# Performance work log

Hardware: AMD Instinct MI355X
Metric: run time of the kernel (lower is better)

## Reference

```python
import jax, jax.numpy as jnp
import numpy as np

N = 50000        # nodes
E = 800000       # edges (avg degree 16)
C_PREV = 256
HID = 256        # C * 4, C = 64
ALPHA = 0.1      # GCNII-style initial-residual weight
LAMBDA = 0.5     # identity-mapping hyperparameter
LAYER = 1
BN_EPS = 1e-5
GIN_EPS = 0.0    # GIN epsilon (default 0)


def setup_inputs() -> dict:
    key = jax.random.key(0)
    ks = jax.random.split(key, 6)
    s0 = jax.random.normal(ks[0], (N, C_PREV), jnp.float32)
    s1 = jax.random.normal(ks[1], (N, C_PREV), jnp.float32)
    x_0 = jax.random.normal(ks[2], (N, HID), jnp.float32)
    # preprocess MLP: Linear(C_prev -> 4C, bias=False) + BatchNorm + ReLU
    W_pre = jax.random.normal(ks[3], (C_PREV, HID), jnp.float32) / np.sqrt(C_PREV).astype(np.float32)
    gamma = jnp.ones((HID,), jnp.float32)
    beta_bn = jnp.zeros((HID,), jnp.float32)
    # ginii op weight (identity-mapped linear, GCNII style)
    W_op = jax.random.normal(ks[4], (HID, HID), jnp.float32) / np.sqrt(HID).astype(np.float32)
    edge_index = jax.random.randint(ks[5], (2, E), 0, N, dtype=jnp.int32)
    return {"s0": s0, "s1": s1, "x_0": x_0, "W_pre": W_pre, "gamma": gamma,
            "beta_bn": beta_bn, "W_op": W_op, "edge_index": edge_index,
            "drop_prob": 0, "training": 0}


def reference(s0, s1, x_0, W_pre, gamma, beta_bn, W_op, edge_index, drop_prob, training):
    # preprocess1: Linear (no bias) -> BatchNorm (batch stats) -> ReLU
    h = s1 @ W_pre                                        # [N, HID]
    mu = h.mean(axis=0)
    var = h.var(axis=0)
    h = (h - mu) * jax.lax.rsqrt(var + BN_EPS) * gamma + beta_bn
    h = jax.nn.relu(h)

    # ginii: GIN-style sum aggregation over edge_index with initial residual
    # and identity-mapped weight (GCNII trick).
    src, dst = edge_index[0], edge_index[1]
    agg = jax.ops.segment_sum(h[src], dst, num_segments=N)   # [N, HID]
    h = (1.0 + GIN_EPS) * h + agg
    support = (1.0 - ALPHA) * h + ALPHA * x_0
    beta = float(np.log(LAMBDA / LAYER + 1.0))
    out = jax.nn.relu((1.0 - beta) * support + beta * (support @ W_op))
    return out
```

## Files before the change

kernel.cpp:

```cpp
#include <hip/hip_runtime.h>

#define NNODES 50000
#define NEDGES 800000
#define HIDDIM 256
#define NCHUNK  1563
#define GEMMB   256
#define DEGCAP  64

constexpr float kAlpha = 0.1f;
constexpr float kBnEps = 1e-5f;
constexpr float kBeta  = 0.40546510810816438198f;

typedef __attribute__((ext_vector_type(8))) short  bf16x8;
typedef __attribute__((ext_vector_type(4))) float  f32x4;

typedef __attribute__((address_space(1))) const unsigned int gu32;
typedef __attribute__((address_space(3))) unsigned int       lu32;

static __device__ __forceinline__ unsigned short f2bf(float f) {
  unsigned u = __float_as_uint(f);
  u = (u + 0x7FFFu + ((u >> 16) & 1u)) >> 16;
  return (unsigned short)u;
}
static __device__ __forceinline__ float bf2f(unsigned short h) {
  return __uint_as_float(((unsigned)h) << 16);
}

static __device__ __forceinline__ void load_B_transpose(
    const float* __restrict__ W, unsigned short* Bl, int t) {
#pragma unroll 4
  for (int i = 0; i < 128; ++i) {
    int idx = i * 512 + t;
    int k = idx >> 8, n = idx & 255;
    unsigned short w = f2bf(W[k * 256 + n]);
    *(unsigned short*)((char*)Bl + n * 512 + ((k * 2) ^ ((n & 7) << 4))) = w;
  }
}

__global__ __launch_bounds__(512) void gemm1_fill_persist_k(
    const float* __restrict__ Ain,
    const float* __restrict__ W_pre,
    unsigned short* __restrict__ Cout,
    float* __restrict__ colsum,
    float* __restrict__ colsumsq,
    const int* __restrict__ ei,
    int* __restrict__ cnt,
    int* __restrict__ esrc,
    int M) {
  __shared__ __align__(16) unsigned short Bl[256 * 256];
  __shared__ __align__(16) unsigned short Al[2][32 * 256];

  const int t    = threadIdx.x;
  const int lane = t & 63;
  const int wid  = t >> 6;
  const int wr   = wid >> 2;
  const int wc   = wid & 3;

  load_B_transpose(W_pre, Bl, t);

  float spart[4] = {0.f, 0.f, 0.f, 0.f};
  float qpart[4] = {0.f, 0.f, 0.f, 0.f};

  auto stageA = [&](int buf, int chunk) {
    const int r0 = chunk * 32;
#pragma unroll
    for (int s = 0; s < 4; ++s) {
      int e   = s * 512 + t;
      int row = e >> 6;
      int c4  = e & 63;
      int arow = r0 + row;
      float4 p = make_float4(0.f, 0.f, 0.f, 0.f);
      if (arow < M) p = *(const float4*)(Ain + (size_t)arow * 256 + c4 * 4);
      short4 v;
      v.x = (short)f2bf(p.x); v.y = (short)f2bf(p.y);
      v.z = (short)f2bf(p.z); v.w = (short)f2bf(p.w);
      char* base = (char*)&Al[buf][0] + row * 512;
      *(short4*)(base + ((c4 * 8) ^ ((row & 7) << 4))) = v;
    }
  };

  stageA(0, blockIdx.x);
  __syncthreads();

  const int4* src4 = (const int4*)ei;
  const int4* dst4 = (const int4*)(ei + NEDGES);
  const int n4 = NEDGES / 4;

  int nc = 0;
  for (int c = blockIdx.x; c < NCHUNK; c += GEMMB, ++nc) {
    const int cur = nc & 1;
    const int cn = c + GEMMB;
    if (cn < NCHUNK) stageA(cur ^ 1, cn);

    if (nc < 2) {
      int i = nc * (GEMMB * 512) + (int)blockIdx.x * 512 + t;
      if (i < n4) {
        int4 s = src4[i];
        int4 d = dst4[i];
        int p;
        p = atomicAdd(&cnt[d.x], 1); if (p < DEGCAP) esrc[d.x * DEGCAP + p] = s.x;
        p = atomicAdd(&cnt[d.y], 1); if (p < DEGCAP) esrc[d.y * DEGCAP + p] = s.y;
        p = atomicAdd(&cnt[d.z], 1); if (p < DEGCAP) esrc[d.z * DEGCAP + p] = s.z;
        p = atomicAdd(&cnt[d.w], 1); if (p < DEGCAP) esrc[d.w * DEGCAP + p] = s.w;
      }
    }

    f32x4 acc[4] = {};
    const int arow_f = wr * 16 + (lane & 15);
    const int asw = (arow_f & 7) << 4;
#pragma unroll
    for (int ks = 0; ks < 8; ++ks) {
      const int koff = ks * 64 + ((lane >> 4) * 16);
      bf16x8 af = *(const bf16x8*)((char*)&Al[cur][0] + arow_f * 512 + (koff ^ asw));
#pragma unroll
      for (int n = 0; n < 4; ++n) {
        int nr = wc * 64 + n * 16 + (lane & 15);
        bf16x8 bfr = *(const bf16x8*)((char*)Bl + (size_t)nr * 512 + (koff ^ ((nr & 7) << 4)));
        acc[n] = __builtin_amdgcn_mfma_f32_16x16x32_bf16(af, bfr, acc[n], 0, 0, 0);
      }
    }

#pragma unroll
    for (int n = 0; n < 4; ++n) {
      int col = wc * 64 + n * 16 + (lane & 15);
      float s = 0.f, q = 0.f;
#pragma unroll
      for (int r = 0; r < 4; ++r) {
        int row = c * 32 + wr * 16 + (lane >> 4) * 4 + r;
        float v = acc[n][r];
        s += v; q += v * v;
        if (row < M) Cout[(size_t)row * 256 + col] = f2bf(v);
      }
      spart[n] += s; qpart[n] += q;
    }
    __syncthreads();
  }

#pragma unroll
  for (int n = 0; n < 4; ++n) {
    float s = spart[n], q = qpart[n];
    s += __shfl_xor(s, 16); s += __shfl_xor(s, 32);
    q += __shfl_xor(q, 16); q += __shfl_xor(q, 32);
    if (lane < 16) {
      int col = wc * 64 + n * 16 + lane;
      atomicAdd(&colsum[col], s);
      atomicAdd(&colsumsq[col], q);
    }
  }
}

__global__ __launch_bounds__(512) void gemm2_persist_k(
    const unsigned short* __restrict__ Ain,
    const float* __restrict__ W_op,
    float* __restrict__ Cout,
    int M) {
  __shared__ __align__(16) unsigned short Bl[256 * 256];
  __shared__ __align__(16) unsigned short Al[2][32 * 256];

  const int t    = threadIdx.x;
  const int lane = t & 63;
  const int wid  = t >> 6;
  const int wr   = wid >> 2;
  const int wc   = wid & 3;

  load_B_transpose(W_op, Bl, t);

  auto stageA = [&](int buf, int chunk) {
    const int lrow = lane >> 5, lchk = lane & 31;
#pragma unroll
    for (int c = 0; c < 2; ++c) {
      int issue = wid * 2 + c;
      int row = issue * 2 + lrow;
      int srcoff = (lchk * 16) ^ ((row & 7) << 4);
      const char* g = (const char*)Ain + (size_t)(chunk * 32 + row) * 512 + srcoff;
      char* l = (char*)&Al[buf][0] + issue * 1024 + lane * 16;
      __builtin_amdgcn_global_load_lds((gu32*)g, (lu32*)l, 16, 0, 0);
    }
  };

  stageA(0, blockIdx.x);
  __syncthreads();

  int nc = 0;
  for (int c = blockIdx.x; c < NCHUNK; c += GEMMB, ++nc) {
    const int cur = nc & 1;
    if (c + GEMMB < NCHUNK) stageA(cur ^ 1, c + GEMMB);

    f32x4 acc[4] = {};
    const int arow_f = wr * 16 + (lane & 15);
    const int asw = (arow_f & 7) << 4;
#pragma unroll
    for (int ks = 0; ks < 8; ++ks) {
      const int koff = ks * 64 + ((lane >> 4) * 16);
      bf16x8 af = *(const bf16x8*)((char*)&Al[cur][0] + arow_f * 512 + (koff ^ asw));
#pragma unroll
      for (int n = 0; n < 4; ++n) {
        int nr = wc * 64 + n * 16 + (lane & 15);
        bf16x8 bfr = *(const bf16x8*)((char*)Bl + (size_t)nr * 512 + (koff ^ ((nr & 7) << 4)));
        acc[n] = __builtin_amdgcn_mfma_f32_16x16x32_bf16(af, bfr, acc[n], 0, 0, 0);
      }
    }

#pragma unroll
    for (int n = 0; n < 4; ++n) {
      int col = wc * 64 + n * 16 + (lane & 15);
#pragma unroll
      for (int r = 0; r < 4; ++r) {
        int rl = wr * 16 + (lane >> 4) * 4 + r;
        int row = c * 32 + rl;
        if (row < M) {
          unsigned short sv = *(const unsigned short*)
              ((char*)&Al[cur][0] + rl * 512 + ((col * 2) ^ ((rl & 7) << 4)));
          Cout[(size_t)row * 256 + col] =
              fmaxf((1.f - kBeta) * bf2f(sv) + kBeta * acc[n][r], 0.f);
        }
      }
    }
    __syncthreads();
  }
}

__global__ __launch_bounds__(256) void agg_bn_support_k(
    const unsigned short* __restrict__ hb,
    const int* __restrict__ cnt,
    const int* __restrict__ esrc,
    const float* __restrict__ x0,
    const float* __restrict__ colsum,
    const float* __restrict__ colsumsq,
    const float* __restrict__ gamma,
    const float* __restrict__ beta_bn,
    unsigned short* __restrict__ supp_bf) {
  __shared__ float s_sc[256], s_sh[256];
  {
    int j = threadIdx.x;
    float inv_n = 1.0f / (float)NNODES;
    float mu  = colsum[j] * inv_n;
    float var = colsumsq[j] * inv_n - mu * mu;
    float rstd = rsqrtf(var + kBnEps);
    float g = gamma[j] * rstd;
    s_sc[j] = g;
    s_sh[j] = beta_bn[j] - mu * g;
  }
  __syncthreads();

  const int hw   = threadIdx.x >> 5;
  const int lane = threadIdx.x & 31;
  const int d    = blockIdx.x * 8 + hw;
  const int off  = lane * 8;

  float sc[8], sh[8];
  *(float4*)&sc[0] = *(const float4*)(s_sc + off);
  *(float4*)&sc[4] = *(const float4*)(s_sc + off + 4);
  *(float4*)&sh[0] = *(const float4*)(s_sh + off);
  *(float4*)&sh[4] = *(const float4*)(s_sh + off + 4);

  const int beg = d * DEGCAP;
  int deg = cnt[d]; if (deg > DEGCAP) deg = DEGCAP;
  const int end = beg + deg;
  float acc[8] = {0.f, 0.f, 0.f, 0.f, 0.f, 0.f, 0.f, 0.f};

  for (int bb = beg; bb < end; bb += 32) {
    int c32 = end - bb; if (c32 > 32) c32 = 32;
    int myi = esrc[bb + ((lane < c32) ? lane : 0)];
    int u = 0;
    for (; u + 3 < c32; u += 4) {
      int s0 = __shfl(myi, u, 32),     s1 = __shfl(myi, u + 1, 32);
      int s2 = __shfl(myi, u + 2, 32), s3 = __shfl(myi, u + 3, 32);
      bf16x8 v0 = *(const bf16x8*)(hb + (size_t)s0 * HIDDIM + off);
      bf16x8 v1 = *(const bf16x8*)(hb + (size_t)s1 * HIDDIM + off);
      bf16x8 v2 = *(const bf16x8*)(hb + (size_t)s2 * HIDDIM + off);
      bf16x8 v3 = *(const bf16x8*)(hb + (size_t)s3 * HIDDIM + off);
#pragma unroll
      for (int j = 0; j < 8; ++j) {
        acc[j] += fmaxf(fmaf(bf2f((unsigned short)v0[j]), sc[j], sh[j]), 0.f)
                + fmaxf(fmaf(bf2f((unsigned short)v1[j]), sc[j], sh[j]), 0.f)
                + fmaxf(fmaf(bf2f((unsigned short)v2[j]), sc[j], sh[j]), 0.f)
                + fmaxf(fmaf(bf2f((unsigned short)v3[j]), sc[j], sh[j]), 0.f);
      }
    }
    for (; u < c32; ++u) {
      int s0 = __shfl(myi, u, 32);
      bf16x8 v0 = *(const bf16x8*)(hb + (size_t)s0 * HIDDIM + off);
#pragma unroll
      for (int j = 0; j < 8; ++j)
        acc[j] += fmaxf(fmaf(bf2f((unsigned short)v0[j]), sc[j], sh[j]), 0.f);
    }
  }

  bf16x8 vd = *(const bf16x8*)(hb + (size_t)d * HIDDIM + off);
  f32x4 xa = __builtin_nontemporal_load((const f32x4*)(x0 + (size_t)d * HIDDIM + off));
  f32x4 xb = __builtin_nontemporal_load((const f32x4*)(x0 + (size_t)d * HIDDIM + off + 4));
  float xs[8] = {xa.x, xa.y, xa.z, xa.w, xb.x, xb.y, xb.z, xb.w};
  bf16x8 o;
#pragma unroll
  for (int j = 0; j < 8; ++j) {
    float hv = fmaxf(fmaf(bf2f((unsigned short)vd[j]), sc[j], sh[j]), 0.f);
    o[j] = (short)f2bf((1.f - kAlpha) * (hv + acc[j]) + kAlpha * xs[j]);
  }
  __builtin_nontemporal_store(o, (bf16x8*)(supp_bf + (size_t)d * HIDDIM + off));
}

extern "C" void kernel_launch(void* const* d_in, const int* in_sizes, int n_in,
                              void* d_out, int out_size, void* d_ws, size_t ws_size,
                              hipStream_t stream) {
  const float* s1    = (const float*)d_in[1];
  const float* x0    = (const float*)d_in[2];
  const float* W_pre = (const float*)d_in[3];
  const float* gamma = (const float*)d_in[4];
  const float* betab = (const float*)d_in[5];
  const float* W_op  = (const float*)d_in[6];
  const int*   ei    = (const int*)d_in[7];
  float* out = (float*)d_out;

  const size_t NH = (size_t)NNODES * HIDDIM;
  unsigned short* hbf   = (unsigned short*)d_ws;
  unsigned short* supbf = hbf + NH;
  int*   cnt      = (int*)(supbf + NH);
  float* colsum   = (float*)(cnt + NNODES);
  float* colsumsq = colsum + HIDDIM;
  int*   esrc     = (int*)(colsumsq + HIDDIM);

  hipMemsetAsync(cnt, 0, (NNODES + 2 * HIDDIM) * sizeof(int), stream);

  gemm1_fill_persist_k<<<GEMMB, 512, 0, stream>>>(s1, W_pre, hbf, colsum, colsumsq,
                                                  ei, cnt, esrc, NNODES);

  agg_bn_support_k<<<(NNODES + 7) / 8, 256, 0, stream>>>(hbf, cnt, esrc, x0,
                                                         colsum, colsumsq, gamma, betab,
                                                         supbf);

  gemm2_persist_k<<<GEMMB, 512, 0, stream>>>(supbf, W_op, out, NNODES);
}
```

Baseline: 174.2 us.

## Split gemm1 into dynamic-scheduled MFMA waves plus dedicated edge-fill warps

Replaces the persistent gemm1 kernel with a 768-thread block in which 8 waves pull 16-row chunks from a global atomic work counter. Each wave loads its A fragments straight from global memory into registers and computes all 256 columns. The other 4 waves do the CSR-style edge bucketing at the same time. Column sums are gathered in LDS atomics before one global atomic per column. The aim is to balance work across blocks, overlap edge filling with the GEMM, and drop the LDS staging of A. The cost is more register pressure (16 accumulators) and no double buffering of A loads.

```diff
diff --git a/kernel.cpp b/kernel.cpp
--- a/kernel.cpp
+++ b/kernel.cpp
@@ -4,6 +4,7 @@
 #define NEDGES 800000
 #define HIDDIM 256
 #define NCHUNK  1563
+#define NCH16   3125
 #define GEMMB   256
 #define DEGCAP  64
 
@@ -24,6 +25,106 @@
 }
 static __device__ __forceinline__ float bf2f(unsigned short h) {
   return __uint_as_float(((unsigned)h) << 16);
+}
+
+__global__ __launch_bounds__(768) void gemm1_fill_k(
+    const float* __restrict__ Ain,
+    const float* __restrict__ W_pre,
+    unsigned short* __restrict__ Cout,
+    float* __restrict__ colsum,
+    float* __restrict__ colsumsq,
+    const int* __restrict__ ei,
+    int* __restrict__ cnt,
+    int* __restrict__ esrc,
+    int* __restrict__ chunkctr) {
+  __shared__ __align__(16) unsigned short Bl[256 * 256];
+  __shared__ float csl[256], cql[256];
+
+  const int t    = threadIdx.x;
+  const int lane = t & 63;
+  const int wid  = t >> 6;
+
+  for (int idx = t; idx < 65536; idx += 768) {
+    int k = idx >> 8, n = idx & 255;
+    unsigned short w = f2bf(W_pre[k * 256 + n]);
+    *(unsigned short*)((char*)Bl + n * 512 + ((k * 2) ^ ((n & 7) << 4))) = w;
+  }
+  if (t < 256) { csl[t] = 0.f; cql[t] = 0.f; }
+  __syncthreads();
+
+  if (wid < 8) {
+    while (true) {
+      int c0;
+      if (lane == 0) c0 = atomicAdd(chunkctr, 1);
+      c0 = __shfl(c0, 0);
+      if (c0 >= NCH16) break;
+
+      const float* ap = Ain + (size_t)(c0 * 16 + (lane & 15)) * 256 + ((lane >> 4) * 8);
+      bf16x8 af[8];
+#pragma unroll
+      for (int ks = 0; ks < 8; ++ks) {
+        float4 p0 = *(const float4*)(ap + ks * 32);
+        float4 p1 = *(const float4*)(ap + ks * 32 + 4);
+        bf16x8 v;
+        v[0] = (short)f2bf(p0.x); v[1] = (short)f2bf(p0.y);
+        v[2] = (short)f2bf(p0.z); v[3] = (short)f2bf(p0.w);
+        v[4] = (short)f2bf(p1.x); v[5] = (short)f2bf(p1.y);
+        v[6] = (short)f2bf(p1.z); v[7] = (short)f2bf(p1.w);
+        af[ks] = v;
+      }
+
+      f32x4 acc[16] = {};
+#pragma unroll
+      for (int ks = 0; ks < 8; ++ks) {
+        const int koff = ks * 64 + ((lane >> 4) * 16);
+#pragma unroll
+        for (int n = 0; n < 16; ++n) {
+          int nr = n * 16 + (lane & 15);
+          bf16x8 bfr = *(const bf16x8*)((char*)Bl + (size_t)nr * 512 + (koff ^ ((nr & 7) << 4)));
+          acc[n] = __builtin_amdgcn_mfma_f32_16x16x32_bf16(af[ks], bfr, acc[n], 0, 0, 0);
+        }
+      }
+
+#pragma unroll
+      for (int n = 0; n < 16; ++n) {
+        int col = n * 16 + (lane & 15);
+        float s = 0.f, q = 0.f;
+#pragma unroll
+        for (int r = 0; r < 4; ++r) {
+          int orow = c0 * 16 + (lane >> 4) * 4 + r;
+          float v = acc[n][r];
+          s += v; q += v * v;
+          Cout[(size_t)orow * 256 + col] = f2bf(v);
+        }
+        s += __shfl_xor(s, 16); s += __shfl_xor(s, 32);
+        q += __shfl_xor(q, 16); q += __shfl_xor(q, 32);
+        if (lane < 16) {
+          atomicAdd(&csl[col], s);
+          atomicAdd(&cql[col], q);
+        }
+      }
+    }
+  } else {
+    const int4* src4 = (const int4*)ei;
+    const int4* dst4 = (const int4*)(ei + NEDGES);
+    const int n4 = NEDGES / 4;
+    int ft = (int)blockIdx.x * 256 + (t - 512);
+    for (int i = ft; i < n4; i += GEMMB * 256) {
+      int4 s = src4[i];
+      int4 d = dst4[i];
+      int p;
+      p = atomicAdd(&cnt[d.x], 1); if (p < DEGCAP) esrc[d.x * DEGCAP + p] = s.x;
+      p = atomicAdd(&cnt[d.y], 1); if (p < DEGCAP) esrc[d.y * DEGCAP + p] = s.y;
+      p = atomicAdd(&cnt[d.z], 1); if (p < DEGCAP) esrc[d.z * DEGCAP + p] = s.z;
+      p = atomicAdd(&cnt[d.w], 1); if (p < DEGCAP) esrc[d.w * DEGCAP + p] = s.w;
+    }
+  }
+
+  __syncthreads();
+  if (t < 256) {
+    atomicAdd(&colsum[t], csl[t]);
+    atomicAdd(&colsumsq[t], cql[t]);
+  }
 }
 
 static __device__ __forceinline__ void load_B_transpose(
@@ -34,118 +135,6 @@
     int k = idx >> 8, n = idx & 255;
     unsigned short w = f2bf(W[k * 256 + n]);
     *(unsigned short*)((char*)Bl + n * 512 + ((k * 2) ^ ((n & 7) << 4))) = w;
-  }
-}
-
-__global__ __launch_bounds__(512) void gemm1_fill_persist_k(
-    const float* __restrict__ Ain,
-    const float* __restrict__ W_pre,
-    unsigned short* __restrict__ Cout,
-    float* __restrict__ colsum,
-    float* __restrict__ colsumsq,
-    const int* __restrict__ ei,
-    int* __restrict__ cnt,
-    int* __restrict__ esrc,
-    int M) {
-  __shared__ __align__(16) unsigned short Bl[256 * 256];
-  __shared__ __align__(16) unsigned short Al[2][32 * 256];
-
-  const int t    = threadIdx.x;
-  const int lane = t & 63;
-  const int wid  = t >> 6;
-  const int wr   = wid >> 2;
-  const int wc   = wid & 3;
-
-  load_B_transpose(W_pre, Bl, t);
-
-  float spart[4] = {0.f, 0.f, 0.f, 0.f};
-  float qpart[4] = {0.f, 0.f, 0.f, 0.f};
-
-  auto stageA = [&](int buf, int chunk) {
-    const int r0 = chunk * 32;
-#pragma unroll
-    for (int s = 0; s < 4; ++s) {
-      int e   = s * 512 + t;
-      int row = e >> 6;
-      int c4  = e & 63;
-      int arow = r0 + row;
-      float4 p = make_float4(0.f, 0.f, 0.f, 0.f);
-      if (arow < M) p = *(const float4*)(Ain + (size_t)arow * 256 + c4 * 4);
-      short4 v;
-      v.x = (short)f2bf(p.x); v.y = (short)f2bf(p.y);
-      v.z = (short)f2bf(p.z); v.w = (short)f2bf(p.w);
-      char* base = (char*)&Al[buf][0] + row * 512;
-      *(short4*)(base + ((c4 * 8) ^ ((row & 7) << 4))) = v;
-    }
-  };
-
-  stageA(0, blockIdx.x);
-  __syncthreads();
-
-  const int4* src4 = (const int4*)ei;
-  const int4* dst4 = (const int4*)(ei + NEDGES);
-  const int n4 = NEDGES / 4;
-
-  int nc = 0;
-  for (int c = blockIdx.x; c < NCHUNK; c += GEMMB, ++nc) {
-    const int cur = nc & 1;
-    const int cn = c + GEMMB;
-    if (cn < NCHUNK) stageA(cur ^ 1, cn);
-
-    if (nc < 2) {
-      int i = nc * (GEMMB * 512) + (int)blockIdx.x * 512 + t;
-      if (i < n4) {
-        int4 s = src4[i];
-        int4 d = dst4[i];
-        int p;
-        p = atomicAdd(&cnt[d.x], 1); if (p < DEGCAP) esrc[d.x * DEGCAP + p] = s.x;
-        p = atomicAdd(&cnt[d.y], 1); if (p < DEGCAP) esrc[d.y * DEGCAP + p] = s.y;
-        p = atomicAdd(&cnt[d.z], 1); if (p < DEGCAP) esrc[d.z * DEGCAP + p] = s.z;
-        p = atomicAdd(&cnt[d.w], 1); if (p < DEGCAP) esrc[d.w * DEGCAP + p] = s.w;
-      }
-    }
-
-    f32x4 acc[4] = {};
-    const int arow_f = wr * 16 + (lane & 15);
-    const int asw = (arow_f & 7) << 4;
-#pragma unroll
-    for (int ks = 0; ks < 8; ++ks) {
-      const int koff = ks * 64 + ((lane >> 4) * 16);
-      bf16x8 af = *(const bf16x8*)((char*)&Al[cur][0] + arow_f * 512 + (koff ^ asw));
-#pragma unroll
-      for (int n = 0; n < 4; ++n) {
-        int nr = wc * 64 + n * 16 + (lane & 15);
-        bf16x8 bfr = *(const bf16x8*)((char*)Bl + (size_t)nr * 512 + (koff ^ ((nr & 7) << 4)));
-        acc[n] = __builtin_amdgcn_mfma_f32_16x16x32_bf16(af, bfr, acc[n], 0, 0, 0);
-      }
-    }
-
-#pragma unroll
-    for (int n = 0; n < 4; ++n) {
-      int col = wc * 64 + n * 16 + (lane & 15);
-      float s = 0.f, q = 0.f;
-#pragma unroll
-      for (int r = 0; r < 4; ++r) {
-        int row = c * 32 + wr * 16 + (lane >> 4) * 4 + r;
-        float v = acc[n][r];
-        s += v; q += v * v;
-        if (row < M) Cout[(size_t)row * 256 + col] = f2bf(v);
-      }
-      spart[n] += s; qpart[n] += q;
-    }
-    __syncthreads();
-  }
-
-#pragma unroll
-  for (int n = 0; n < 4; ++n) {
-    float s = spart[n], q = qpart[n];
-    s += __shfl_xor(s, 16); s += __shfl_xor(s, 32);
-    q += __shfl_xor(q, 16); q += __shfl_xor(q, 32);
-    if (lane < 16) {
-      int col = wc * 64 + n * 16 + lane;
-      atomicAdd(&colsum[col], s);
-      atomicAdd(&colsumsq[col], q);
-    }
   }
 }
 
@@ -318,12 +307,13 @@
   int*   cnt      = (int*)(supbf + NH);
   float* colsum   = (float*)(cnt + NNODES);
   float* colsumsq = colsum + HIDDIM;
-  int*   esrc     = (int*)(colsumsq + HIDDIM);
-
-  hipMemsetAsync(cnt, 0, (NNODES + 2 * HIDDIM) * sizeof(int), stream);
-
-  gemm1_fill_persist_k<<<GEMMB, 512, 0, stream>>>(s1, W_pre, hbf, colsum, colsumsq,
-                                                  ei, cnt, esrc, NNODES);
+  int*   chunkctr = (int*)(colsumsq + HIDDIM);
+  int*   esrc     = chunkctr + 1;
+
+  hipMemsetAsync(cnt, 0, (NNODES + 2 * HIDDIM + 1) * sizeof(int), stream);
+
+  gemm1_fill_k<<<GEMMB, 768, 0, stream>>>(s1, W_pre, hbf, colsum, colsumsq,
+                                          ei, cnt, esrc, chunkctr);
 
   agg_bn_support_k<<<(NNODES + 7) / 8, 256, 0, stream>>>(hbf, cnt, esrc, x0,
                                                          colsum, colsumsq, gamma, betab,
```

Result: slower. 209.9 us (+20.5%).
